# Optimization experiments

Hardware: AMD Instinct MI355X
Metric: run time of the kernel (lower is better)

Reference implementation:

```python
import jax, jax.numpy as jnp
import numpy as np

H = 16      # num_heads
W = 256     # one_sided_attn_window_size
S = 4096    # seq_len (multiple of 2*W as Longformer requires)
D = 1024    # embed_dim
B = 1       # batch (the module's squeeze() calls assume batch == 1)


def setup_inputs() -> dict:
    key = jax.random.key(0)
    ks = jax.random.split(key, 4)
    sc = 1.0 / float(np.sqrt(D))
    return {
        "hidden_states": jax.random.normal(ks[0], (B, S, D), jnp.float32),
        "attention_mask": jnp.zeros((B, S), jnp.float32),   # 0 = local attention everywhere
        "is_index_masked": jnp.zeros((B, S), jnp.bool_),
        "Wq": jax.random.normal(ks[1], (D, D), jnp.float32) * sc,
        "bq": jnp.zeros((D,), jnp.float32),
        "Wk": jax.random.normal(ks[2], (D, D), jnp.float32) * sc,
        "bk": jnp.zeros((D,), jnp.float32),
        "Wv": jax.random.normal(ks[3], (D, D), jnp.float32) * sc,
        "bv": jnp.zeros((D,), jnp.float32),
    }


def _forward(hidden_states, attention_mask, is_index_masked, Wq, bq, Wk, bk, Wv, bv):
    d = D // H                     # head_dim
    C = S // W                     # number of query chunks of width W

    def heads(x):                  # [B,S,D] -> [B,H,S,d]
        return x.reshape(B, S, H, d).transpose(0, 2, 1, 3)

    q = heads(hidden_states @ Wq.T + bq) * (1.0 / float(np.sqrt(d)))
    k = heads(hidden_states @ Wk.T + bk)
    # mca.simple_mca is an unbiased randomized Monte-Carlo estimator of the exact
    # value projection; the exact linear is the deterministic reference for its math.
    v = heads(hidden_states @ Wv.T + bv)

    # sliding-chunks: query chunk c attends to zero-padded keys [c*W, c*W + 3W)
    kp = jnp.pad(k, ((0, 0), (0, 0), (W, W), (0, 0)))
    vp = jnp.pad(v, ((0, 0), (0, 0), (W, W), (0, 0)))
    ci = jnp.arange(C)[:, None] * W + jnp.arange(3 * W)[None, :]   # [C, 3W]
    kc = kp[:, :, ci]                                              # [B,H,C,3W,d]
    vc = vp[:, :, ci]                                              # [B,H,C,3W,d]
    qc = q.reshape(B, H, C, W, d)
    sc_ = jnp.einsum('bhcxd,bhcyd->bhcxy', qc, kc)                 # [B,H,C,W,3W]

    # extract the 2W+1 diagonal band: key offset within chunk for (x, j) is x + j
    xa = jnp.arange(W)[:, None]          # [W,1]
    ja = jnp.arange(2 * W + 1)[None, :]  # [1,2W+1]
    band = sc_[:, :, :, xa, xa + ja].reshape(B, H, S, 2 * W + 1)

    # mask invalid (out-of-sequence) diagonals and add the float attention mask,
    # gathered along the same band (equivalent to HF's diagonal_mask trick)
    pos = jnp.arange(S)[:, None] - W + ja            # global key index per (i, j)
    valid = (pos >= 0) & (pos < S)                   # [S, 2W+1]
    float_mask = jnp.where(attention_mask != 0, -10000.0, 0.0)          # [B,S]
    fm = jnp.where(valid[None], float_mask[:, jnp.clip(pos, 0, S - 1)], 0.0)
    scores = band + fm[:, None]                                         # [B,H,S,2W+1]
    scores = jnp.where(valid[None, None], scores, jnp.finfo(scores.dtype).min)

    probs = jax.nn.softmax(scores.astype(jnp.float32), axis=-1)
    probs = jnp.where(is_index_masked[:, None, :, None], 0.0, probs).astype(scores.dtype)
    # dropout p with training=False is identity

    # scatter band probs back into per-chunk [W, 3W] layout, contract with values
    pc = probs.reshape(B, H, C, W, 2 * W + 1)
    full = jnp.zeros((B, H, C, W, 3 * W), probs.dtype).at[:, :, :, xa, xa + ja].set(pc)
    out = jnp.einsum('bhcxy,bhcyd->bhcxd', full, vc)                    # [B,H,C,W,d]
    return out.reshape(B, H, S, d).transpose(0, 2, 1, 3).reshape(B, S, D)


def reference(hidden_states, attention_mask, is_index_masked, Wq, bq, Wk, bk, Wv, bv):
    return _forward(hidden_states, attention_mask, is_index_masked, Wq, bq, Wk, bk, Wv, bv)
```

## Files before the change

### kernel.cpp

```cpp
#include <hip/hip_runtime.h>
#include <hip/hip_bf16.h>

typedef unsigned short u16;
typedef __attribute__((ext_vector_type(8))) __bf16 bf16x8;
typedef __attribute__((ext_vector_type(8))) unsigned short u16x8;
typedef __attribute__((ext_vector_type(4))) float f32x4;
typedef __attribute__((ext_vector_type(4))) unsigned short u16x4;

#define SEQ 4096
#define DIM 1024
#define NH 16
#define HD 64
#define WIN 256
#define NT32 (SEQ / 32)
#define NKT 32
#define BQ 128

__device__ inline u16 f2bf(float f) {
  __hip_bfloat16 h = __float2bfloat16(f);
  return __builtin_bit_cast(u16, h);
}

__device__ inline void gload_lds16(const void* g, void* l) {
  auto gp = reinterpret_cast<__attribute__((address_space(1))) unsigned int*>(
      reinterpret_cast<unsigned long long>(g));
  auto lp = reinterpret_cast<__attribute__((address_space(3))) unsigned int*>(
      reinterpret_cast<unsigned long long>(l));
  __builtin_amdgcn_global_load_lds(gp, lp, 16, 0, 0);
}

__global__ __launch_bounds__(256) void cast4(const float* __restrict__ in,
                                             u16* __restrict__ out, int n) {
  int i = (blockIdx.x * 256 + threadIdx.x) * 4;
  if (i >= n) return;
  const float4 v = *reinterpret_cast<const float4*>(in + i);
  u16x4 r;
  r.x = f2bf(v.x); r.y = f2bf(v.y); r.z = f2bf(v.z); r.w = f2bf(v.w);
  *reinterpret_cast<u16x4*>(out + i) = r;
}

__global__ __launch_bounds__(256) void cast_w3(const float* __restrict__ w0, const float* __restrict__ w1,
                                               const float* __restrict__ w2, u16* __restrict__ out) {
  int i = (blockIdx.x * 256 + threadIdx.x) * 4;
  const int seg = i >> 20;
  const int loc = i & ((1 << 20) - 1);
  const float* src = (seg == 0) ? w0 : (seg == 1) ? w1 : w2;
  const float4 v = *reinterpret_cast<const float4*>(src + loc);
  u16x4 r;
  r.x = f2bf(v.x); r.y = f2bf(v.y); r.z = f2bf(v.z); r.w = f2bf(v.w);
  *reinterpret_cast<u16x4*>(out + i) = r;
}

__global__ __launch_bounds__(256) void pack_aux(const float* __restrict__ b0, const float* __restrict__ b1,
                                                const float* __restrict__ b2, const float* __restrict__ amask,
                                                float* __restrict__ out) {
  int i = blockIdx.x * 256 + threadIdx.x;
  if (i < 3072) {
    const int seg = i >> 10, loc = i & 1023;
    out[i] = (seg == 0) ? b0[loc] : (seg == 1) ? b1[loc] : b2[loc];
  } else {
    const int j = i - 3072;
    out[i] = (amask[j] != 0.f) ? -14426.95f : 0.f;
  }
}

__device__ __forceinline__ void stage_tile(const u16* __restrict__ A, const u16* __restrict__ B,
                                           int bm, int bn, u16* sa, u16* sb, int kt, int tid) {
  const int k0 = kt * 32;
#pragma unroll
  for (int l = 0; l < 2; ++l) {
    const int li = l * 512 + tid;
    const int r = li >> 2, c = (li & 3) * 8;
    gload_lds16(A + (size_t)(bm + r) * DIM + k0 + c, sa + li * 8);
    gload_lds16(B + (size_t)(bn + r) * DIM + k0 + c, sb + li * 8);
  }
}

__global__ __launch_bounds__(512, 2) void gemm_qkv(const u16* __restrict__ A, const u16* __restrict__ B,
                                                   const float* __restrict__ bias,
                                                   u16* __restrict__ Qh, u16* __restrict__ Kh,
                                                   u16* __restrict__ Vtile) {
  __shared__ __align__(16) u16 SA[3][256 * 32];
  __shared__ __align__(16) u16 SB[3][256 * 32];
  const int nwgx = gridDim.x;
  const int orig = blockIdx.y * nwgx + blockIdx.x;
  const int cpx = (nwgx * gridDim.y) >> 3;
  const int wgid = (orig & 7) * cpx + (orig >> 3);
  const int bm = (wgid / nwgx) * 256, bn = (wgid % nwgx) * 256;
  const int tid = threadIdx.x;
  const int lane = tid & 63, wid = tid >> 6;
  const int lrow = lane & 15, lgrp = lane >> 4;
  const int wr = (wid >> 2) * 128, wc = (wid & 3) * 64;

  f32x4 acc[8][4];
  const f32x4 zero = {0.f, 0.f, 0.f, 0.f};
#pragma unroll
  for (int m = 0; m < 8; ++m)
#pragma unroll
    for (int n = 0; n < 4; ++n) acc[m][n] = zero;

  stage_tile(A, B, bm, bn, SA[0], SB[0], 0, tid);
  stage_tile(A, B, bm, bn, SA[1], SB[1], 1, tid);
  asm volatile("s_waitcnt vmcnt(4)" ::: "memory");
  asm volatile("s_barrier" ::: "memory");

  for (int t = 0; t < NKT; ++t) {
    const int s = t % 3;
    if (t + 2 < NKT) stage_tile(A, B, bm, bn, SA[(t + 2) % 3], SB[(t + 2) % 3], t + 2, tid);
    bf16x8 af[8], bfr[4];
#pragma unroll
    for (int m = 0; m < 8; ++m)
      af[m] = *reinterpret_cast<const bf16x8*>(&SA[s][(wr + m * 16 + lrow) * 32 + lgrp * 8]);
#pragma unroll
    for (int n = 0; n < 4; ++n)
      bfr[n] = *reinterpret_cast<const bf16x8*>(&SB[s][(wc + n * 16 + lrow) * 32 + lgrp * 8]);
    __builtin_amdgcn_s_setprio(1);
#pragma unroll
    for (int m = 0; m < 8; ++m)
#pragma unroll
      for (int n = 0; n < 4; ++n)
        acc[m][n] = __builtin_amdgcn_mfma_f32_16x16x32_bf16(af[m], bfr[n], acc[m][n], 0, 0, 0);
    __builtin_amdgcn_s_setprio(0);
    if (t + 2 < NKT) { asm volatile("s_waitcnt vmcnt(4)" ::: "memory"); }
    else if (t + 1 < NKT) { asm volatile("s_waitcnt vmcnt(0)" ::: "memory"); }
    asm volatile("s_barrier" ::: "memory");
  }

#pragma unroll
  for (int m = 0; m < 8; ++m)
#pragma unroll
    for (int n = 0; n < 4; ++n) {
      const int row0 = bm + wr + m * 16 + lgrp * 4;
      const int colg = bn + wc + n * 16 + lrow;
      const float b = bias[colg];
      if (bn < 2048) {
        u16* dst = (bn < 1024) ? Qh : Kh;
        const float sc = (bn < 1024) ? 0.18033688f : 1.0f;
        const int hh = (colg & 1023) >> 6;
        const int dd = colg & 63;
#pragma unroll
        for (int r = 0; r < 4; ++r)
          dst[((size_t)hh * SEQ + row0 + r) * HD + dd] = f2bf((acc[m][n][r] + b) * sc);
      } else {
        const int dv = colg - 2048;
        const int hh = dv >> 6, dd = dv & 63;
        const int k5 = row0 & 31;
        const int pos = (k5 < 16) ? ((k5 >> 2) * 8) : (((k5 - 16) >> 2) * 8 + 4);
        u16x4 pk;
#pragma unroll
        for (int r = 0; r < 4; ++r) pk[r] = f2bf(acc[m][n][r] + b);
        u16* vt = Vtile + ((((size_t)hh * NT32 + (row0 >> 5)) * HD + dd) << 5) + pos;
        *reinterpret_cast<u16x4*>(vt) = pk;
      }
    }
}

__global__ __launch_bounds__(512) void lf_attn(const u16* __restrict__ Qh, const u16* __restrict__ Kh,
                                               const u16* __restrict__ Vtile, const float* __restrict__ fm,
                                               float* __restrict__ out) {
  const int nwgx = gridDim.x;
  const int nwg = nwgx * gridDim.y;
  const int orig = blockIdx.y * nwgx + blockIdx.x;
  const int cpx = nwg >> 3;
  const int wgid = (orig & 7) * cpx + (orig >> 3);
  const int h = wgid / nwgx;
  const int q0 = (wgid % nwgx) * BQ;
  const int tid = threadIdx.x;
  const int wid = tid >> 6, lane = tid & 63;
  const int lrow = lane & 15, lgrp = lane >> 4;
  const int qw = q0 + wid * 16;

  __shared__ __align__(16) u16 KL[3][32 * HD];
  __shared__ __align__(16) u16 VL[3][HD * 32];

  bf16x8 qf0, qf1;
  {
    const u16* qbase = Qh + ((size_t)h * SEQ + qw + lrow) * HD + lgrp * 8;
    qf0 = *reinterpret_cast<const bf16x8*>(qbase);
    qf1 = *reinterpret_cast<const bf16x8*>(qbase + 32);
  }
  const f32x4 zero = {0.f, 0.f, 0.f, 0.f};
  f32x4 o_acc[4];
  float psum = 0.f;
#pragma unroll
  for (int g = 0; g < 4; ++g) o_acc[g] = zero;

  int kstart = q0 - WIN; if (kstart < 0) kstart = 0; kstart &= ~31;
  int kend = q0 + BQ - 1 + WIN + 1; if (kend > SEQ) kend = SEQ;
  const int NTT = (kend - kstart) >> 5;

  const int q_abs = qw + lrow;

  auto stage = [&](int t, int buf) {
    const int kt = kstart + t * 32;
    if (tid < 256) {
      const int row = tid >> 3, slot = tid & 7;
      const u16* src = Kh + ((size_t)h * SEQ + kt + row) * HD + ((slot ^ (row & 7)) * 8);
      gload_lds16(src, &KL[buf][tid * 8]);
    } else {
      const int c = tid - 256;
      const int row = c >> 2, slot = c & 3;
      const u16* src = Vtile + ((size_t)h * NT32 + (kt >> 5)) * (HD * 32) + row * 32 + ((slot ^ (row & 3)) * 8);
      gload_lds16(src, &VL[buf][c * 8]);
    }
  };

  stage(0, 0);
  stage(1, 1);
  asm volatile("s_waitcnt vmcnt(1)" ::: "memory");
  asm volatile("s_barrier" ::: "memory");

  for (int t = 0; t < NTT; ++t) {
    const int s = t % 3;
    if (t + 2 < NTT) stage(t + 2, (t + 2) % 3);
    const int kt = kstart + t * 32;
    const bool active = (kt + 31 >= qw - WIN) && (kt <= qw + 15 + WIN);
    if (active) {
      const int xk = (lrow & 7) * 8;
      const int xv = (lrow & 3) * 8;
      const u16* KB = &KL[s][0];
      const u16* VB = &VL[s][0];
      const bf16x8 kf0 = *reinterpret_cast<const bf16x8*>(KB + lrow * 64        + (((lgrp)     * 8) ^ xk));
      const bf16x8 kf1 = *reinterpret_cast<const bf16x8*>(KB + lrow * 64        + (((lgrp + 4) * 8) ^ xk));
      const bf16x8 kf2 = *reinterpret_cast<const bf16x8*>(KB + (16 + lrow) * 64 + (((lgrp)     * 8) ^ xk));
      const bf16x8 kf3 = *reinterpret_cast<const bf16x8*>(KB + (16 + lrow) * 64 + (((lgrp + 4) * 8) ^ xk));
      const bf16x8 vf0 = *reinterpret_cast<const bf16x8*>(VB + lrow * 32        + ((lgrp * 8) ^ xv));
      const bf16x8 vf1 = *reinterpret_cast<const bf16x8*>(VB + (16 + lrow) * 32 + ((lgrp * 8) ^ xv));
      const bf16x8 vf2 = *reinterpret_cast<const bf16x8*>(VB + (32 + lrow) * 32 + ((lgrp * 8) ^ xv));
      const bf16x8 vf3 = *reinterpret_cast<const bf16x8*>(VB + (48 + lrow) * 32 + ((lgrp * 8) ^ xv));

      f32x4 s0 = zero, s1 = zero;
      s0 = __builtin_amdgcn_mfma_f32_16x16x32_bf16(kf0, qf0, s0, 0, 0, 0);
      s0 = __builtin_amdgcn_mfma_f32_16x16x32_bf16(kf1, qf1, s0, 0, 0, 0);
      s1 = __builtin_amdgcn_mfma_f32_16x16x32_bf16(kf2, qf0, s1, 0, 0, 0);
      s1 = __builtin_amdgcn_mfma_f32_16x16x32_bf16(kf3, qf1, s1, 0, 0, 0);

      const float4 f0 = *reinterpret_cast<const float4*>(fm + kt + lgrp * 4);
      const float4 f1 = *reinterpret_cast<const float4*>(fm + kt + 16 + lgrp * 4);
      const float f0v[4] = {f0.x, f0.y, f0.z, f0.w};
      const float f1v[4] = {f1.x, f1.y, f1.z, f1.w};

      u16x8 pu;
      if (kt >= qw - 241 && kt <= qw + 225) {
#pragma unroll
        for (int r = 0; r < 4; ++r) {
          const float e0 = __builtin_amdgcn_exp2f(s0[r] + f0v[r]);
          const float e1 = __builtin_amdgcn_exp2f(s1[r] + f1v[r]);
          psum += e0 + e1;
          pu[r] = f2bf(e0);
          pu[4 + r] = f2bf(e1);
        }
      } else {
#pragma unroll
        for (int r = 0; r < 4; ++r) {
          const int key0 = kt + lgrp * 4 + r;
          const int d0 = key0 - q_abs + WIN;
          const float e0 = ((unsigned)d0 <= 2u * WIN) ? __builtin_amdgcn_exp2f(s0[r] + f0v[r]) : 0.f;
          const float e1 = ((unsigned)(d0 + 16) <= 2u * WIN) ? __builtin_amdgcn_exp2f(s1[r] + f1v[r]) : 0.f;
          psum += e0 + e1;
          pu[r] = f2bf(e0);
          pu[4 + r] = f2bf(e1);
        }
      }
      const bf16x8 pa = __builtin_bit_cast(bf16x8, pu);
      o_acc[0] = __builtin_amdgcn_mfma_f32_16x16x32_bf16(pa, vf0, o_acc[0], 0, 0, 0);
      o_acc[1] = __builtin_amdgcn_mfma_f32_16x16x32_bf16(pa, vf1, o_acc[1], 0, 0, 0);
      o_acc[2] = __builtin_amdgcn_mfma_f32_16x16x32_bf16(pa, vf2, o_acc[2], 0, 0, 0);
      o_acc[3] = __builtin_amdgcn_mfma_f32_16x16x32_bf16(pa, vf3, o_acc[3], 0, 0, 0);
    }
    if (t + 2 < NTT) { asm volatile("s_waitcnt vmcnt(1)" ::: "memory"); }
    else if (t + 1 < NTT) { asm volatile("s_waitcnt vmcnt(0)" ::: "memory"); }
    asm volatile("s_barrier" ::: "memory");
  }

  psum += __shfl_xor(psum, 16);
  psum += __shfl_xor(psum, 32);

  float psr[4];
#pragma unroll
  for (int r = 0; r < 4; ++r) psr[r] = __shfl(psum, lgrp * 4 + r, 64);
#pragma unroll
  for (int g = 0; g < 4; ++g)
#pragma unroll
    for (int r = 0; r < 4; ++r) {
      const int row = qw + lgrp * 4 + r;
      out[(size_t)row * DIM + h * HD + g * 16 + lrow] = o_acc[g][r] / psr[r];
    }
}

extern "C" void kernel_launch(void* const* d_in, const int* in_sizes, int n_in,
                              void* d_out, int out_size, void* d_ws, size_t ws_size,
                              hipStream_t stream) {
  const float* hsrc  = (const float*)d_in[0];
  const float* amask = (const float*)d_in[1];
  const float* Wq = (const float*)d_in[3];
  const float* bq = (const float*)d_in[4];
  const float* Wk = (const float*)d_in[5];
  const float* bk = (const float*)d_in[6];
  const float* Wv = (const float*)d_in[7];
  const float* bv = (const float*)d_in[8];
  float* out = (float*)d_out;
  char* ws = (char*)d_ws;
  const size_t MB = 1024 * 1024;
  u16*   Hb      = (u16*)(ws);
  u16*   Wcat    = (u16*)(ws + 8 * MB);
  float* auxbuf  = (float*)(ws + 14 * MB);
  u16*   Qh      = (u16*)(ws + 15 * MB);
  u16*   Kh      = (u16*)(ws + 23 * MB);
  u16*   Vtile   = (u16*)(ws + 31 * MB);

  cast4<<<4096, 256, 0, stream>>>(hsrc, Hb, SEQ * DIM);
  cast_w3<<<3072, 256, 0, stream>>>(Wq, Wk, Wv, Wcat);
  pack_aux<<<28, 256, 0, stream>>>(bq, bk, bv, amask, auxbuf);

  dim3 gq(3 * DIM / 256, SEQ / 256);
  gemm_qkv<<<gq, 512, 0, stream>>>(Hb, Wcat, auxbuf, Qh, Kh, Vtile);

  dim3 ga(SEQ / BQ, NH);
  lf_attn<<<ga, 512, 0, stream>>>(Qh, Kh, Vtile, auxbuf + 3072, out);
}
```

Before: 76.17 us.

## Shrink QKV GEMM tiles to 128x128, swizzle LDS, fuse cast kernels

The QKV projection GEMM moves from 256x256 tiles with 512 threads to 128x128 tiles with 256 threads. The grid grows from 192 to 768 workgroups, which fills the CUs better, and launch bounds allow three blocks per CU. LDS staging now uses an XOR-swizzled layout that pairs rows, aiming to cut bank conflicts on fragment reads. The two fp32-to-bf16 cast kernels are merged into one launch to save a kernel launch. The trade-off is less operand reuse per tile, so global and L2 traffic goes up.

```diff
diff --git a/kernel.cpp b/kernel.cpp
--- a/kernel.cpp
+++ b/kernel.cpp
@@ -29,26 +29,24 @@
   __builtin_amdgcn_global_load_lds(gp, lp, 16, 0, 0);
 }
 
-__global__ __launch_bounds__(256) void cast4(const float* __restrict__ in,
-                                             u16* __restrict__ out, int n) {
+__global__ __launch_bounds__(256) void cast_all(const float* __restrict__ hsrc,
+                                                const float* __restrict__ w0, const float* __restrict__ w1,
+                                                const float* __restrict__ w2,
+                                                u16* __restrict__ Hb, u16* __restrict__ Wcat) {
   int i = (blockIdx.x * 256 + threadIdx.x) * 4;
-  if (i >= n) return;
-  const float4 v = *reinterpret_cast<const float4*>(in + i);
+  const float* src;
+  u16* dst;
+  if (i < (1 << 22)) { src = hsrc + i; dst = Hb + i; }
+  else {
+    int j = i - (1 << 22);
+    const int seg = j >> 20, loc = j & ((1 << 20) - 1);
+    src = ((seg == 0) ? w0 : (seg == 1) ? w1 : w2) + loc;
+    dst = Wcat + j;
+  }
+  const float4 v = *reinterpret_cast<const float4*>(src);
   u16x4 r;
   r.x = f2bf(v.x); r.y = f2bf(v.y); r.z = f2bf(v.z); r.w = f2bf(v.w);
-  *reinterpret_cast<u16x4*>(out + i) = r;
-}
-
-__global__ __launch_bounds__(256) void cast_w3(const float* __restrict__ w0, const float* __restrict__ w1,
-                                               const float* __restrict__ w2, u16* __restrict__ out) {
-  int i = (blockIdx.x * 256 + threadIdx.x) * 4;
-  const int seg = i >> 20;
-  const int loc = i & ((1 << 20) - 1);
-  const float* src = (seg == 0) ? w0 : (seg == 1) ? w1 : w2;
-  const float4 v = *reinterpret_cast<const float4*>(src + loc);
-  u16x4 r;
-  r.x = f2bf(v.x); r.y = f2bf(v.y); r.z = f2bf(v.z); r.w = f2bf(v.w);
-  *reinterpret_cast<u16x4*>(out + i) = r;
+  *reinterpret_cast<u16x4*>(dst) = r;
 }
 
 __global__ __launch_bounds__(256) void pack_aux(const float* __restrict__ b0, const float* __restrict__ b1,
@@ -64,59 +62,67 @@
   }
 }
 
-__device__ __forceinline__ void stage_tile(const u16* __restrict__ A, const u16* __restrict__ B,
-                                           int bm, int bn, u16* sa, u16* sb, int kt, int tid) {
+__device__ __forceinline__ void stage_tile128(const u16* __restrict__ A, const u16* __restrict__ B,
+                                              int bm, int bn, u16* sa, u16* sb, int kt, int tid) {
   const int k0 = kt * 32;
 #pragma unroll
   for (int l = 0; l < 2; ++l) {
-    const int li = l * 512 + tid;
-    const int r = li >> 2, c = (li & 3) * 8;
-    gload_lds16(A + (size_t)(bm + r) * DIM + k0 + c, sa + li * 8);
-    gload_lds16(B + (size_t)(bn + r) * DIM + k0 + c, sb + li * 8);
-  }
-}
-
-__global__ __launch_bounds__(512, 2) void gemm_qkv(const u16* __restrict__ A, const u16* __restrict__ B,
+    const int u = l * 256 + tid;
+    const int sr = u >> 3, half = (u >> 2) & 1, sp = u & 3;
+    const int row = sr * 2 + half;
+    const int slot = sp ^ (sr & 3);
+    gload_lds16(A + (size_t)(bm + row) * DIM + k0 + slot * 8, sa + u * 8);
+    gload_lds16(B + (size_t)(bn + row) * DIM + k0 + slot * 8, sb + u * 8);
+  }
+}
+
+__global__ __launch_bounds__(256, 3) void gemm_qkv(const u16* __restrict__ A, const u16* __restrict__ B,
                                                    const float* __restrict__ bias,
                                                    u16* __restrict__ Qh, u16* __restrict__ Kh,
                                                    u16* __restrict__ Vtile) {
-  __shared__ __align__(16) u16 SA[3][256 * 32];
-  __shared__ __align__(16) u16 SB[3][256 * 32];
+  __shared__ __align__(16) u16 SA[3][128 * 32];
+  __shared__ __align__(16) u16 SB[3][128 * 32];
   const int nwgx = gridDim.x;
   const int orig = blockIdx.y * nwgx + blockIdx.x;
   const int cpx = (nwgx * gridDim.y) >> 3;
   const int wgid = (orig & 7) * cpx + (orig >> 3);
-  const int bm = (wgid / nwgx) * 256, bn = (wgid % nwgx) * 256;
+  const int bm = (wgid / nwgx) * 128, bn = (wgid % nwgx) * 128;
   const int tid = threadIdx.x;
   const int lane = tid & 63, wid = tid >> 6;
   const int lrow = lane & 15, lgrp = lane >> 4;
-  const int wr = (wid >> 2) * 128, wc = (wid & 3) * 64;
-
-  f32x4 acc[8][4];
+  const int wr = (wid >> 1) * 64, wc = (wid & 1) * 64;
+
+  f32x4 acc[4][4];
   const f32x4 zero = {0.f, 0.f, 0.f, 0.f};
 #pragma unroll
-  for (int m = 0; m < 8; ++m)
+  for (int m = 0; m < 4; ++m)
 #pragma unroll
     for (int n = 0; n < 4; ++n) acc[m][n] = zero;
 
-  stage_tile(A, B, bm, bn, SA[0], SB[0], 0, tid);
-  stage_tile(A, B, bm, bn, SA[1], SB[1], 1, tid);
+  stage_tile128(A, B, bm, bn, SA[0], SB[0], 0, tid);
+  stage_tile128(A, B, bm, bn, SA[1], SB[1], 1, tid);
   asm volatile("s_waitcnt vmcnt(4)" ::: "memory");
   asm volatile("s_barrier" ::: "memory");
 
   for (int t = 0; t < NKT; ++t) {
     const int s = t % 3;
-    if (t + 2 < NKT) stage_tile(A, B, bm, bn, SA[(t + 2) % 3], SB[(t + 2) % 3], t + 2, tid);
-    bf16x8 af[8], bfr[4];
-#pragma unroll
-    for (int m = 0; m < 8; ++m)
-      af[m] = *reinterpret_cast<const bf16x8*>(&SA[s][(wr + m * 16 + lrow) * 32 + lgrp * 8]);
-#pragma unroll
-    for (int n = 0; n < 4; ++n)
-      bfr[n] = *reinterpret_cast<const bf16x8*>(&SB[s][(wc + n * 16 + lrow) * 32 + lgrp * 8]);
+    if (t + 2 < NKT) stage_tile128(A, B, bm, bn, SA[(t + 2) % 3], SB[(t + 2) % 3], t + 2, tid);
+    bf16x8 af[4], bfr[4];
+#pragma unroll
+    for (int m = 0; m < 4; ++m) {
+      const int row = wr + m * 16 + lrow;
+      af[m] = *reinterpret_cast<const bf16x8*>(
+          &SA[s][(row >> 1) * 64 + (row & 1) * 32 + ((lgrp ^ ((row >> 1) & 3)) * 8)]);
+    }
+#pragma unroll
+    for (int n = 0; n < 4; ++n) {
+      const int row = wc + n * 16 + lrow;
+      bfr[n] = *reinterpret_cast<const bf16x8*>(
+          &SB[s][(row >> 1) * 64 + (row & 1) * 32 + ((lgrp ^ ((row >> 1) & 3)) * 8)]);
+    }
     __builtin_amdgcn_s_setprio(1);
 #pragma unroll
-    for (int m = 0; m < 8; ++m)
+    for (int m = 0; m < 4; ++m)
 #pragma unroll
       for (int n = 0; n < 4; ++n)
         acc[m][n] = __builtin_amdgcn_mfma_f32_16x16x32_bf16(af[m], bfr[n], acc[m][n], 0, 0, 0);
@@ -127,7 +133,7 @@
   }
 
 #pragma unroll
-  for (int m = 0; m < 8; ++m)
+  for (int m = 0; m < 4; ++m)
 #pragma unroll
     for (int n = 0; n < 4; ++n) {
       const int row0 = bm + wr + m * 16 + lgrp * 4;
@@ -309,12 +315,11 @@
   u16*   Kh      = (u16*)(ws + 23 * MB);
   u16*   Vtile   = (u16*)(ws + 31 * MB);
 
-  cast4<<<4096, 256, 0, stream>>>(hsrc, Hb, SEQ * DIM);
-  cast_w3<<<3072, 256, 0, stream>>>(Wq, Wk, Wv, Wcat);
+  cast_all<<<7168, 256, 0, stream>>>(hsrc, Wq, Wk, Wv, Hb, Wcat);
   pack_aux<<<28, 256, 0, stream>>>(bq, bk, bv, amask, auxbuf);
 
-  dim3 gq(3 * DIM / 256, SEQ / 256);
-  gemm_qkv<<<gq, 512, 0, stream>>>(Hb, Wcat, auxbuf, Qh, Kh, Vtile);
+  dim3 gq(3 * DIM / 128, SEQ / 128);
+  gemm_qkv<<<gq, 256, 0, stream>>>(Hb, Wcat, auxbuf, Qh, Kh, Vtile);
 
   dim3 ga(SEQ / BQ, NH);
   lf_attn<<<ga, 512, 0, stream>>>(Qh, Kh, Vtile, auxbuf + 3072, out);
```

After: 72.47 us. 4.9% less time.
